# Kernel tuning notes

Hardware: AMD Instinct MI355X
Metric: run time of the kernel (lower is better)

## Reference

```python
import jax, jax.numpy as jnp
import numpy as np

B, S, D, H, HD = 2, 2048, 1024, 16, 64
LN_EPS = 1e-6


def setup_inputs() -> dict:
    key = jax.random.key(0)
    ks = jax.random.split(key, 4)
    x = jax.random.normal(ks[0], (B, S, D), dtype=jnp.float32)
    ln_scale = jnp.ones((D,), jnp.float32)
    ln_bias = jnp.zeros((D,), jnp.float32)
    w_qkv = jax.random.normal(ks[1], (D, H, 3 * HD), jnp.float32) * (D ** -0.5)
    b_qkv = jnp.zeros((H, 3 * HD), jnp.float32)
    w_out = jax.random.normal(ks[2], (H, HD, D), jnp.float32) * ((H * HD) ** -0.5)
    b_out = jnp.zeros((D,), jnp.float32)
    # causal mask, broadcastable to weights shape [B, H, q, k]
    mask = jnp.tril(jnp.ones((S, S), dtype=bool))[None, None, :, :]
    return {"x": x, "ln_scale": ln_scale, "ln_bias": ln_bias,
            "w_qkv": w_qkv, "b_qkv": b_qkv, "w_out": w_out, "b_out": b_out,
            "mask": mask}


def _attention_block(x, ln_scale, ln_bias, w_qkv, b_qkv, w_out, b_out, mask):
    # Pre-LayerNorm
    mu = jnp.mean(x, axis=-1, keepdims=True)
    var = jnp.mean(jnp.square(x - mu), axis=-1, keepdims=True)
    xn = (x - mu) * jax.lax.rsqrt(var + LN_EPS) * ln_scale + ln_bias
    # QKV projection: [B,S,D] x [D,H,3*hd] -> [B,S,H,3*hd]
    qkv = jnp.einsum('bsd,dhf->bshf', xn, w_qkv) + b_qkv
    q, k, v = jnp.split(qkv, 3, axis=-1)  # each [B,S,H,hd]
    # scaled dot-product attention in float32 (softmax_dtype)
    scale = HD ** -0.5
    qf = (q * scale).astype(jnp.float32)
    kf = k.astype(jnp.float32)
    weights = jnp.einsum('bqhd,bkhd->bhqk', qf, kf)  # [B,H,S,S]
    weights = jnp.where(mask, weights, jnp.finfo(jnp.float32).min)
    weights = jax.nn.softmax(weights, axis=-1).astype(x.dtype)
    attn = jnp.einsum('bhqk,bkhd->bqhd', weights, v)  # [B,S,H,hd]
    # output projection, contracting (H, hd)
    out = jnp.einsum('bqhd,hdf->bqf', attn, w_out) + b_out  # [B,S,D]
    return out


def reference(x, ln_scale, ln_bias, w_qkv, b_qkv, w_out, b_out, mask):
    return _attention_block(x, ln_scale, ln_bias, w_qkv, b_qkv, w_out, b_out, mask)
```

## Files before the change

kernel.cpp:

```cpp
#include <hip/hip_runtime.h>
#include <hip/hip_bf16.h>
#include <stdint.h>

#define B_ 2
#define S_ 2048
#define D_ 1024
#define H_ 16
#define HD_ 64
#define M_ (B_*S_)
#define NQKV_ (H_*3*HD_)

typedef __attribute__((ext_vector_type(8))) short short8;
typedef __attribute__((ext_vector_type(4))) float f32x4;
typedef unsigned short u16;
typedef unsigned int u32;

__device__ __forceinline__ u16 f2b(float f){
  u32 u = __float_as_uint(f);
  u32 r = (u + 0x7FFFu + ((u >> 16) & 1u)) >> 16;
  return (u16)r;
}

__device__ __forceinline__ float exp2v(float x){
  float r; asm("v_exp_f32 %0, %1" : "=v"(r) : "v"(x)); return r;
}

__device__ __forceinline__ void gl_lds16(const void* g, void* l){
  __builtin_amdgcn_global_load_lds(
      (const __attribute__((address_space(1))) void*)g,
      (__attribute__((address_space(3))) void*)l, 16, 0, 0);
}

__global__ __launch_bounds__(256) void prep_kernel(
    const float* __restrict__ x, const float* __restrict__ gam,
    const float* __restrict__ bet, u16* __restrict__ xn,
    const float* __restrict__ wqkv, u16* __restrict__ wqkvT,
    const float* __restrict__ wout, u16* __restrict__ woutT){
  int bid = blockIdx.x;
  __shared__ float tile[64][65];
  if(bid < M_){
    int row = bid;
    const float4* xr = (const float4*)(x + (size_t)row * D_);
    float4 v = xr[threadIdx.x];
    float s = v.x + v.y + v.z + v.w;
    float q = v.x*v.x + v.y*v.y + v.z*v.z + v.w*v.w;
    #pragma unroll
    for(int o = 32; o > 0; o >>= 1){ s += __shfl_down(s, o); q += __shfl_down(q, o); }
    float* red = &tile[0][0];
    int w = threadIdx.x >> 6, lane = threadIdx.x & 63;
    if(lane == 0){ red[w] = s; red[4+w] = q; }
    __syncthreads();
    float st = red[0]+red[1]+red[2]+red[3];
    float qt = red[4]+red[5]+red[6]+red[7];
    float mu = st * (1.0f / D_);
    float inv = rsqrtf(qt * (1.0f / D_) - mu*mu + 1e-6f);
    float4 g = ((const float4*)gam)[threadIdx.x];
    float4 b = ((const float4*)bet)[threadIdx.x];
    ushort4 o4;
    o4.x = f2b((v.x-mu)*inv*g.x + b.x);
    o4.y = f2b((v.y-mu)*inv*g.y + b.y);
    o4.z = f2b((v.z-mu)*inv*g.z + b.z);
    o4.w = f2b((v.w-mu)*inv*g.w + b.w);
    ((ushort4*)(xn + (size_t)row * D_))[threadIdx.x] = o4;
    return;
  }
  const float* src; u16* dst; int C, cx, ry;
  if(bid < M_ + (NQKV_/64)*(D_/64)){
    int idx = bid - M_;
    cx = idx % (NQKV_/64); ry = idx / (NQKV_/64);
    src = wqkv; dst = wqkvT; C = NQKV_;
  } else {
    int idx = bid - M_ - (NQKV_/64)*(D_/64);
    cx = idx % (D_/64); ry = idx / (D_/64);
    src = wout; dst = woutT; C = D_;
  }
  const int R = D_;
  int tx = threadIdx.x & 63, ty = threadIdx.x >> 6;
  int r0 = ry * 64, c0 = cx * 64;
  #pragma unroll
  for(int i = 0; i < 16; i++){
    int r = ty*16 + i;
    tile[r][tx] = src[(size_t)(r0+r)*C + c0 + tx];
  }
  __syncthreads();
  #pragma unroll
  for(int i = 0; i < 16; i++){
    int r = ty*16 + i;
    dst[(size_t)(c0+r)*R + r0 + tx] = f2b(tile[tx][r]);
  }
}

__global__ __launch_bounds__(512, 1) void gemm256_kernel(const u16* __restrict__ A,
    const u16* __restrict__ Bt, const float* __restrict__ bias,
    u16* __restrict__ o0, u16* __restrict__ o1, u16* __restrict__ o2t){
  constexpr int K_ = 1024;
  __shared__ __align__(16) char smem[114688];
  int tid = threadIdx.x, w = tid >> 6, lane = tid & 63;
  int wm = w >> 1, wn = w & 1;
  int bid = blockIdx.y * gridDim.x + blockIdx.x;
  int nwg = gridDim.x * gridDim.y;
  int cpx = nwg >> 3;
  int swz = (bid & 7) * cpx + (bid >> 3);
  int m0 = (swz / gridDim.x) * 256, n0 = (swz % gridDim.x) * 192;

  f32x4 z = {0.f, 0.f, 0.f, 0.f};
  f32x4 acc[4][6];
  #pragma unroll
  for(int r = 0; r < 4; r++)
    #pragma unroll
    for(int c = 0; c < 6; c++) acc[r][c] = z;

  int srow8 = tid >> 3;
  int sch = (tid & 7) ^ (srow8 & 7);
  auto STAGE_A = [&](int buf, int half, int kt){
    #pragma unroll
    for(int l = 0; l < 2; l++){
      int row = half*128 + l*64 + srow8;
      gl_lds16(A + (size_t)(m0 + row)*K_ + kt*64 + sch*8,
               smem + buf*32768 + half*16384 + l*8192 + tid*16);
    }
  };
  auto STAGE_B3 = [&](int slot, int third, int kt){
    int row = third*64 + srow8;
    gl_lds16(Bt + (size_t)(n0 + row)*K_ + kt*64 + sch*8,
             smem + 65536 + slot*24576 + third*8192 + tid*16);
  };

  int ln15 = lane & 15, g = lane >> 4;
  int co0 = ((g    ) ^ (ln15 & 7)) * 16;
  int co1 = ((4 + g) ^ (ln15 & 7)) * 16;
  auto LDA = [&](int buf, int r, int k)->short8{
    int row = wm*64 + r*16 + ln15;
    return *(const short8*)(smem + buf*32768 + row*128 + (k ? co1 : co0));
  };
  auto LDB = [&](int slot, int c, int k)->short8{
    int row = wn*96 + c*16 + ln15;
    return *(const short8*)(smem + 65536 + slot*24576 + row*128 + (k ? co1 : co0));
  };
  #define BAR()   __builtin_amdgcn_s_barrier()
  #define LGKM0() do{ asm volatile("s_waitcnt lgkmcnt(0)" ::: "memory"); \
                      __builtin_amdgcn_sched_barrier(0); }while(0)
  #define MF(r_, c_, a_, b_) acc[r_][c_] = __builtin_amdgcn_mfma_f32_16x16x32_bf16(a_, b_, acc[r_][c_], 0, 0, 0)

  constexpr int nk = K_ / 64;
  STAGE_A(0, 0, 0); STAGE_A(0, 1, 0);
  STAGE_B3(0, 0, 0); STAGE_B3(0, 1, 0); STAGE_B3(0, 2, 0);
  STAGE_B3(1, 0, 1); STAGE_B3(1, 1, 1); STAGE_B3(1, 2, 1);
  asm volatile("s_waitcnt vmcnt(3)" ::: "memory");
  __builtin_amdgcn_sched_barrier(0);
  BAR();

  #pragma unroll 2
  for(int t = 0; t < nk; t++){
    int buf = t & 1;
    int kA = (t + 1 < nk) ? t + 1 : nk - 1;
    int kB = (t + 2 < nk) ? t + 2 : nk - 1;
    short8 a[4][2], b01[2][2], b23[2][2], b45[2][2];
    #pragma unroll
    for(int r = 0; r < 4; r++){ a[r][0] = LDA(buf, r, 0); a[r][1] = LDA(buf, r, 1); }
    #pragma unroll
    for(int c = 0; c < 2; c++){ b01[c][0] = LDB(buf, c, 0); b01[c][1] = LDB(buf, c, 1); }
    STAGE_A(buf ^ 1, 0, kA);
    BAR(); LGKM0();
    __builtin_amdgcn_s_setprio(1);
    #pragma unroll
    for(int r = 0; r < 4; r++)
      #pragma unroll
      for(int c = 0; c < 2; c++){ MF(r, c, a[r][0], b01[c][0]); MF(r, c, a[r][1], b01[c][1]); }
    __builtin_amdgcn_s_setprio(0);
    BAR();
    #pragma unroll
    for(int c = 0; c < 2; c++){ b23[c][0] = LDB(buf, c + 2, 0); b23[c][1] = LDB(buf, c + 2, 1); }
    STAGE_A(buf ^ 1, 1, kA);
    BAR(); LGKM0();
    __builtin_amdgcn_s_setprio(1);
    #pragma unroll
    for(int r = 0; r < 4; r++)
      #pragma unroll
      for(int c = 0; c < 2; c++){ MF(r, c+2, a[r][0], b23[c][0]); MF(r, c+2, a[r][1], b23[c][1]); }
    __builtin_amdgcn_s_setprio(0);
    BAR();
    #pragma unroll
    for(int c = 0; c < 2; c++){ b45[c][0] = LDB(buf, c + 4, 0); b45[c][1] = LDB(buf, c + 4, 1); }
    BAR(); LGKM0();
    __builtin_amdgcn_s_setprio(1);
    #pragma unroll
    for(int r = 0; r < 4; r++){ MF(r, 4, a[r][0], b45[0][0]); MF(r, 4, a[r][1], b45[0][1]); }
    __builtin_amdgcn_s_setprio(0);
    BAR();
    STAGE_B3(buf, 0, kB); STAGE_B3(buf, 1, kB); STAGE_B3(buf, 2, kB);
    BAR();
    __builtin_amdgcn_s_setprio(1);
    #pragma unroll
    for(int r = 0; r < 4; r++){ MF(r, 5, a[r][0], b45[1][0]); MF(r, 5, a[r][1], b45[1][1]); }
    __builtin_amdgcn_s_setprio(0);
    asm volatile("s_waitcnt vmcnt(3)" ::: "memory");
    __builtin_amdgcn_sched_barrier(0);
    BAR();
  }
  #undef BAR
  #undef LGKM0
  #undef MF

  int h = n0 / 192;
  #pragma unroll
  for(int r = 0; r < 4; r++){
    #pragma unroll
    for(int c = 0; c < 6; c++){
      #pragma unroll
      for(int q = 0; q < 4; q++){
        int row = m0 + wm*64 + r*16 + g*4 + q;
        int rr = wn*96 + c*16 + ln15;
        float v = acc[r][c][q] + bias[h*192 + rr];
        int b = row >> 11, s = row & (S_ - 1);
        if(rr < 64){
          o0[((size_t)(b*H_ + h)*S_ + s)*HD_ + rr] = f2b(v * 0.180336884f);
        } else if(rr < 128){
          o1[((size_t)(b*H_ + h)*S_ + s)*HD_ + rr - 64] = f2b(v);
        } else {
          o2t[((size_t)(b*H_ + h)*HD_ + rr - 128)*S_ + s] = f2b(v);
        }
      }
    }
  }
}

__global__ __launch_bounds__(256) void gemm_kernel(const u16* __restrict__ A,
    const u16* __restrict__ Bt, const float* __restrict__ bias,
    float* __restrict__ out, int K, int N){
  __shared__ u16 As[2][128*32];
  __shared__ u16 Bs[2][128*32];
  int tid = threadIdx.x, w = tid >> 6, lane = tid & 63;
  int bid = blockIdx.y * gridDim.x + blockIdx.x;
  int nwg = gridDim.x * gridDim.y;
  int cpx = nwg >> 3;
  int swz = (bid & 7) * cpx + (bid >> 3);
  int m0 = (swz / gridDim.x) * 128, n0 = (swz % gridDim.x) * 128;
  int wm = w >> 1, wn = w & 1;
  f32x4 z = {0.f, 0.f, 0.f, 0.f};
  f32x4 acc[4][4];
  #pragma unroll
  for(int r = 0; r < 4; r++)
    #pragma unroll
    for(int c = 0; c < 4; c++) acc[r][c] = z;
  int srow = lane >> 2, sch = (lane & 3) * 8;
  const u16* Ag = A + (size_t)m0 * K + (size_t)srow * K + sch;
  const u16* Bg = Bt + (size_t)n0 * K + (size_t)srow * K + sch;

  auto STAGE = [&](int buf, int kt){
    #pragma unroll
    for(int i = 0; i < 2; i++){
      int rb = w*32 + i*16;
      gl_lds16(Ag + (size_t)rb*K + kt, &As[buf][rb*32]);
      gl_lds16(Bg + (size_t)rb*K + kt, &Bs[buf][rb*32]);
    }
  };

  int nk = K >> 5;
  STAGE(0, 0);
  asm volatile("s_waitcnt vmcnt(0)" ::: "memory");
  __builtin_amdgcn_sched_barrier(0);
  __builtin_amdgcn_s_barrier();
  for(int t = 0; t < nk; t++){
    int cur = t & 1;
    if(t + 1 < nk){
      STAGE(cur ^ 1, (t + 1) * 32);
      asm volatile("s_waitcnt vmcnt(4)" ::: "memory");
    } else {
      asm volatile("s_waitcnt vmcnt(0)" ::: "memory");
    }
    __builtin_amdgcn_sched_barrier(0);
    __builtin_amdgcn_s_barrier();
    int kc = (lane >> 4) * 8;
    int ar = wm*64 + (lane & 15);
    int bc = wn*64 + (lane & 15);
    short8 af[4], bfr[4];
    #pragma unroll
    for(int r = 0; r < 4; r++) af[r] = *(const short8*)&As[cur][(ar + r*16)*32 + kc];
    #pragma unroll
    for(int c = 0; c < 4; c++) bfr[c] = *(const short8*)&Bs[cur][(bc + c*16)*32 + kc];
    __builtin_amdgcn_s_setprio(1);
    #pragma unroll
    for(int r = 0; r < 4; r++)
      #pragma unroll
      for(int c = 0; c < 4; c++)
        acc[r][c] = __builtin_amdgcn_mfma_f32_16x16x32_bf16(af[r], bfr[c], acc[r][c], 0, 0, 0);
    __builtin_amdgcn_s_setprio(0);
    asm volatile("" ::: "memory");
    __builtin_amdgcn_s_barrier();
  }

  #pragma unroll
  for(int r = 0; r < 4; r++){
    #pragma unroll
    for(int c = 0; c < 4; c++){
      #pragma unroll
      for(int q = 0; q < 4; q++){
        int row = m0 + wm*64 + r*16 + (lane >> 4)*4 + q;
        int col = n0 + wn*64 + c*16 + (lane & 15);
        out[(size_t)row * N + col] = acc[r][c][q] + bias[col];
      }
    }
  }
}


template<int HALF>
__device__ __forceinline__ void compute_tile(
    const char* KsB, const char* VsB, char* Pw, const short8* qf,
    f32x4* o, float& m_run, float& l_run, bool diag, int lane, int wr){
  constexpr int KB0 = (HALF == 1) ? 2 : 0;
  constexpr int KBN = (HALF == -1) ? 4 : 2;
  f32x4 z = {0.f, 0.f, 0.f, 0.f};
  f32x4 sf[4];
  __builtin_amdgcn_s_setprio(1);
  #pragma unroll
  for(int kb = KB0; kb < KB0 + KBN; kb++){
    f32x4 acc = z;
    #pragma unroll
    for(int c = 0; c < 2; c++){
      int row = kb*16 + (lane & 15);
      int kc16 = (lane >> 4) + c*4;
      short8 kf = *(const short8*)(KsB + row*128 + ((kc16 ^ (row & 7)) * 16));
      acc = __builtin_amdgcn_mfma_f32_16x16x32_bf16(kf, qf[c], acc, 0, 0, 0);
    }
    sf[kb] = acc;
  }
  __builtin_amdgcn_s_setprio(0);
  if(diag){
    int qo = wr*16 + (lane & 15);
    #pragma unroll
    for(int kb = KB0; kb < KB0 + KBN; kb++)
      #pragma unroll
      for(int r = 0; r < 4; r++){
        int kvo = kb*16 + (lane >> 4)*4 + r;
        if(kvo > qo) sf[kb][r] = -1e30f;
      }
  }
  int g = lane >> 4;
  float pmax = -1e28f;
  #pragma unroll
  for(int kb = KB0; kb < KB0 + KBN; kb++)
    pmax = fmaxf(pmax, fmaxf(fmaxf(sf[kb][0], sf[kb][1]), fmaxf(sf[kb][2], sf[kb][3])));
  pmax = fmaxf(pmax, __shfl_xor(pmax, 16));
  pmax = fmaxf(pmax, __shfl_xor(pmax, 32));
  if(!__all(pmax <= m_run + 8.f)){
    float mn = fmaxf(m_run, pmax);
    float al = exp2v(m_run - mn);
    m_run = mn;
    l_run *= al;
    float alr[4];
    #pragma unroll
    for(int r = 0; r < 4; r++) alr[r] = __shfl(al, g*4 + r);
    #pragma unroll
    for(int n = 0; n < 4; n++)
      #pragma unroll
      for(int r = 0; r < 4; r++) o[n][r] *= alr[r];
  }
  float p[4][4];
  float sum = 0.f;
  #pragma unroll
  for(int kb = KB0; kb < KB0 + KBN; kb++){
    #pragma unroll
    for(int r = 0; r < 4; r++) p[kb][r] = exp2v(sf[kb][r] - m_run);
    sum += (p[kb][0]+p[kb][1]) + (p[kb][2]+p[kb][3]);
  }
  sum += __shfl_xor(sum, 16);
  sum += __shfl_xor(sum, 32);
  l_run += sum;
  int qrow = lane & 15;
  #pragma unroll
  for(int kb = KB0; kb < KB0 + KBN; kb++){
    u32 lo, hi;
    asm("v_cvt_pk_bf16_f32 %0, %1, %2" : "=v"(lo) : "v"(p[kb][0]), "v"(p[kb][1]));
    asm("v_cvt_pk_bf16_f32 %0, %1, %2" : "=v"(hi) : "v"(p[kb][2]), "v"(p[kb][3]));
    uint2 pk; pk.x = lo; pk.y = hi;
    int byt = (qrow*128 + kb*32 + g*8) ^ ((qrow & 7) << 4);
    *(uint2*)(Pw + byt) = pk;
  }
  constexpr int C0 = (HALF == 1) ? 1 : 0;
  constexpr int C1 = (HALF == 0) ? 0 : 1;
  __builtin_amdgcn_s_setprio(1);
  #pragma unroll
  for(int c = C0; c <= C1; c++){
    int prow = lane & 15;
    int kb16 = ((lane >> 4) + c*4) * 16;
    short8 pa = *(const short8*)(Pw + ((prow*128 + kb16) ^ ((prow & 7) << 4)));
    #pragma unroll
    for(int n = 0; n < 4; n++){
      int vrow = n*16 + (lane & 15);
      int kc16 = (lane >> 4) + c*4;
      short8 vf = *(const short8*)(VsB + vrow*128 + ((kc16 ^ (vrow & 7)) * 16));
      o[n] = __builtin_amdgcn_mfma_f32_16x16x32_bf16(pa, vf, o[n], 0, 0, 0);
    }
  }
  __builtin_amdgcn_s_setprio(0);
}

__global__ __launch_bounds__(512) void attn_kernel(const u16* __restrict__ Q,
    const u16* __restrict__ Kb, const u16* __restrict__ Vt, u16* __restrict__ O){
  __shared__ __align__(16) char smem[49152];
  char* PsBase = smem + 32768;
  int tid = threadIdx.x, w = tid >> 6, lane = tid & 63;
  int wr = w & 3, role = w >> 2;
  int L = blockIdx.x;
  int pi = (L >> 3) & 15;
  int bh = (L & 7) + 8 * (L >> 7);
  const int NT = S_ / 64;
  int ta = pi, tb = NT - 1 - pi;
  const u16* Qg = Q + (size_t)bh * S_ * HD_;
  const u16* Kg = Kb + (size_t)bh * S_ * HD_;
  const u16* Vg = Vt + (size_t)bh * HD_ * S_;
  int b = bh >> 4, h = bh & 15;

  short8 qb[2], qa[2];
  {
    int rb_ = tb*64 + wr*16 + (lane & 15);
    #pragma unroll
    for(int c = 0; c < 2; c++)
      qb[c] = *(const short8*)(Qg + (size_t)rb_*HD_ + (lane >> 4)*8 + c*32);
    if(role == 1){
      int ra_ = ta*64 + wr*16 + (lane & 15);
      #pragma unroll
      for(int c = 0; c < 2; c++)
        qa[c] = *(const short8*)(Qg + (size_t)ra_*HD_ + (lane >> 4)*8 + c*32);
    }
  }
  f32x4 z = {0.f, 0.f, 0.f, 0.f};
  f32x4 o[4];
  float m_run = -1e30f, l_run = 0.f;
  #pragma unroll
  for(int i = 0; i < 4; i++) o[i] = z;
  int svrow = lane >> 3, scb = lane & 7;

  auto STAGE = [&](int buf, int kt){
    int kv0 = kt * 64;
    int rowblk = w * 8;
    int row = rowblk + svrow;
    int cbs = scb ^ (row & 7);
    gl_lds16(Kg + (size_t)(kv0 + row)*HD_ + cbs*8, smem + buf*8192 + rowblk*128);
    gl_lds16(Vg + (size_t)row*S_ + kv0 + cbs*8, smem + 16384 + buf*8192 + rowblk*128);
  };

  STAGE(0, 0);
  asm volatile("s_waitcnt vmcnt(0)" ::: "memory");
  __builtin_amdgcn_sched_barrier(0);
  __builtin_amdgcn_s_barrier();
  int cur = 0;
  char* Pw = PsBase + w*2048;
  for(int kt = 0; kt <= tb; kt++){
    if(kt < tb){
      STAGE(cur ^ 1, kt + 1);
      asm volatile("s_waitcnt vmcnt(2)" ::: "memory");
    } else {
      asm volatile("s_waitcnt vmcnt(0)" ::: "memory");
    }
    __builtin_amdgcn_sched_barrier(0);
    __builtin_amdgcn_s_barrier();
    const char* KsB = (const char*)(smem + cur*8192);
    const char* VsB = (const char*)(smem + 16384 + cur*8192);
    if(role == 0){
      if(kt <= ta) compute_tile<-1>(KsB, VsB, Pw, qb, o, m_run, l_run, false, lane, wr);
      else         compute_tile<0>(KsB, VsB, Pw, qb, o, m_run, l_run, kt == tb, lane, wr);
    } else {
      if(kt <= ta){
        compute_tile<-1>(KsB, VsB, Pw, qa, o, m_run, l_run, kt == ta, lane, wr);
        if(kt == ta){
          float linv = 1.f / l_run;
          float invr[4];
          #pragma unroll
          for(int r = 0; r < 4; r++) invr[r] = __shfl(linv, (lane >> 4)*4 + r);
          #pragma unroll
          for(int n = 0; n < 4; n++)
            #pragma unroll
            for(int r = 0; r < 4; r++){
              int s = ta*64 + wr*16 + (lane >> 4)*4 + r;
              int hd = n*16 + (lane & 15);
              O[(((size_t)(b*S_ + s))*H_ + h)*HD_ + hd] = f2b(o[n][r] * invr[r]);
            }
          m_run = -1e30f; l_run = 0.f;
          #pragma unroll
          for(int i = 0; i < 4; i++) o[i] = z;
        }
      } else {
        compute_tile<1>(KsB, VsB, Pw, qb, o, m_run, l_run, kt == tb, lane, wr);
      }
    }
    asm volatile("" ::: "memory");
    __builtin_amdgcn_s_barrier();
    cur ^= 1;
  }

  float* Mg = (float*)smem + wr*1072;
  if(role == 1){
    #pragma unroll
    for(int n = 0; n < 4; n++)
      #pragma unroll
      for(int r = 0; r < 4; r++)
        Mg[((lane >> 4)*4 + r)*65 + n*16 + (lane & 15)] = o[n][r];
    if(lane < 16){ Mg[1040 + lane] = m_run; Mg[1056 + lane] = l_run; }
  }
  __syncthreads();
  if(role == 0){
    float F1[4], F2[4], den[4];
    #pragma unroll
    for(int r = 0; r < 4; r++){
      int row = (lane >> 4)*4 + r;
      float m1r = __shfl(m_run, row);
      float l1r = __shfl(l_run, row);
      float m2r = Mg[1040 + row];
      float l2r = Mg[1056 + row];
      float mm = fmaxf(m1r, m2r);
      F1[r] = exp2v(m1r - mm);
      F2[r] = exp2v(m2r - mm);
      den[r] = 1.f / (l1r*F1[r] + l2r*F2[r]);
    }
    #pragma unroll
    for(int n = 0; n < 4; n++)
      #pragma unroll
      for(int r = 0; r < 4; r++){
        int row = (lane >> 4)*4 + r;
        float o2 = Mg[row*65 + n*16 + (lane & 15)];
        float val = (o[n][r]*F1[r] + o2*F2[r]) * den[r];
        int s = tb*64 + wr*16 + row;
        int hd = n*16 + (lane & 15);
        O[(((size_t)(b*S_ + s))*H_ + h)*HD_ + hd] = f2b(val);
      }
  }
}

extern "C" void kernel_launch(void* const* d_in, const int* in_sizes, int n_in,
                              void* d_out, int out_size, void* d_ws, size_t ws_size,
                              hipStream_t stream){
  (void)in_sizes; (void)n_in; (void)out_size; (void)ws_size;
  const float* x    = (const float*)d_in[0];
  const float* gam  = (const float*)d_in[1];
  const float* bet  = (const float*)d_in[2];
  const float* wqkv = (const float*)d_in[3];
  const float* bqkv = (const float*)d_in[4];
  const float* wout = (const float*)d_in[5];
  const float* bout = (const float*)d_in[6];
  char* ws = (char*)d_ws;
  u16* xn    = (u16*)(ws);
  u16* wqkvT = (u16*)(ws + 8388608);
  u16* woutT = (u16*)(ws + 8388608 + 6291456);
  u16* Qb    = (u16*)(ws + 16777216);
  u16* Kb    = (u16*)(ws + 16777216 + 8388608);
  u16* Vt    = (u16*)(ws + 16777216 + 2*8388608);
  u16* attnb = xn;
  float* out = (float*)d_out;

  prep_kernel<<<dim3(M_ + (NQKV_/64)*(D_/64) + (D_/64)*(D_/64)), dim3(256), 0, stream>>>(
      x, gam, bet, xn, wqkv, wqkvT, wout, woutT);
  gemm256_kernel<<<dim3(NQKV_/192, M_/256), dim3(512), 0, stream>>>(xn, wqkvT, bqkv, Qb, Kb, Vt);
  attn_kernel<<<dim3(512), dim3(512), 0, stream>>>(Qb, Kb, Vt, attnb);
  gemm_kernel<<<dim3(D_/128, M_/128), dim3(256), 0, stream>>>(attnb, woutT, bout, out, D_, D_);
}
```

Baseline: 115.3 us.

## Replace paired causal q-tile blocks with one q-tile per block, split KV halves

The attention kernel no longer pairs a short and a long causal query tile per block. Each block now handles a single 64-row query tile, with the two wave groups splitting every 64-key KV tile into halves, and the grid doubles to 1024 blocks. Blocks are ordered longest-first, so dynamic scheduling has to do the load balancing. This removes the mid-loop epilogue and the divergent role logic, but it loads each KV tile once per query tile instead of once per pair and halves the MFMA work per barrier.

```diff
diff --git a/kernel.cpp b/kernel.cpp
--- a/kernel.cpp
+++ b/kernel.cpp
@@ -310,12 +310,11 @@
     const char* KsB, const char* VsB, char* Pw, const short8* qf,
     f32x4* o, float& m_run, float& l_run, bool diag, int lane, int wr){
   constexpr int KB0 = (HALF == 1) ? 2 : 0;
-  constexpr int KBN = (HALF == -1) ? 4 : 2;
   f32x4 z = {0.f, 0.f, 0.f, 0.f};
   f32x4 sf[4];
   __builtin_amdgcn_s_setprio(1);
   #pragma unroll
-  for(int kb = KB0; kb < KB0 + KBN; kb++){
+  for(int kb = KB0; kb < KB0 + 2; kb++){
     f32x4 acc = z;
     #pragma unroll
     for(int c = 0; c < 2; c++){
@@ -330,7 +329,7 @@
   if(diag){
     int qo = wr*16 + (lane & 15);
     #pragma unroll
-    for(int kb = KB0; kb < KB0 + KBN; kb++)
+    for(int kb = KB0; kb < KB0 + 2; kb++)
       #pragma unroll
       for(int r = 0; r < 4; r++){
         int kvo = kb*16 + (lane >> 4)*4 + r;
@@ -340,7 +339,7 @@
   int g = lane >> 4;
   float pmax = -1e28f;
   #pragma unroll
-  for(int kb = KB0; kb < KB0 + KBN; kb++)
+  for(int kb = KB0; kb < KB0 + 2; kb++)
     pmax = fmaxf(pmax, fmaxf(fmaxf(sf[kb][0], sf[kb][1]), fmaxf(sf[kb][2], sf[kb][3])));
   pmax = fmaxf(pmax, __shfl_xor(pmax, 16));
   pmax = fmaxf(pmax, __shfl_xor(pmax, 32));
@@ -360,7 +359,7 @@
   float p[4][4];
   float sum = 0.f;
   #pragma unroll
-  for(int kb = KB0; kb < KB0 + KBN; kb++){
+  for(int kb = KB0; kb < KB0 + 2; kb++){
     #pragma unroll
     for(int r = 0; r < 4; r++) p[kb][r] = exp2v(sf[kb][r] - m_run);
     sum += (p[kb][0]+p[kb][1]) + (p[kb][2]+p[kb][3]);
@@ -370,7 +369,7 @@
   l_run += sum;
   int qrow = lane & 15;
   #pragma unroll
-  for(int kb = KB0; kb < KB0 + KBN; kb++){
+  for(int kb = KB0; kb < KB0 + 2; kb++){
     u32 lo, hi;
     asm("v_cvt_pk_bf16_f32 %0, %1, %2" : "=v"(lo) : "v"(p[kb][0]), "v"(p[kb][1]));
     asm("v_cvt_pk_bf16_f32 %0, %1, %2" : "=v"(hi) : "v"(p[kb][2]), "v"(p[kb][3]));
@@ -378,11 +377,9 @@
     int byt = (qrow*128 + kb*32 + g*8) ^ ((qrow & 7) << 4);
     *(uint2*)(Pw + byt) = pk;
   }
-  constexpr int C0 = (HALF == 1) ? 1 : 0;
-  constexpr int C1 = (HALF == 0) ? 0 : 1;
   __builtin_amdgcn_s_setprio(1);
-  #pragma unroll
-  for(int c = C0; c <= C1; c++){
+  {
+    constexpr int c = HALF;
     int prow = lane & 15;
     int kb16 = ((lane >> 4) + c*4) * 16;
     short8 pa = *(const short8*)(Pw + ((prow*128 + kb16) ^ ((prow & 7) << 4)));
@@ -404,27 +401,19 @@
   int tid = threadIdx.x, w = tid >> 6, lane = tid & 63;
   int wr = w & 3, role = w >> 2;
   int L = blockIdx.x;
-  int pi = (L >> 3) & 15;
-  int bh = (L & 7) + 8 * (L >> 7);
-  const int NT = S_ / 64;
-  int ta = pi, tb = NT - 1 - pi;
+  int qt = 31 - (L >> 5);
+  int bh = (L & 7) + 8 * ((L >> 3) & 3);
   const u16* Qg = Q + (size_t)bh * S_ * HD_;
   const u16* Kg = Kb + (size_t)bh * S_ * HD_;
   const u16* Vg = Vt + (size_t)bh * HD_ * S_;
   int b = bh >> 4, h = bh & 15;
 
-  short8 qb[2], qa[2];
+  short8 qf[2];
   {
-    int rb_ = tb*64 + wr*16 + (lane & 15);
+    int rq = qt*64 + wr*16 + (lane & 15);
     #pragma unroll
     for(int c = 0; c < 2; c++)
-      qb[c] = *(const short8*)(Qg + (size_t)rb_*HD_ + (lane >> 4)*8 + c*32);
-    if(role == 1){
-      int ra_ = ta*64 + wr*16 + (lane & 15);
-      #pragma unroll
-      for(int c = 0; c < 2; c++)
-        qa[c] = *(const short8*)(Qg + (size_t)ra_*HD_ + (lane >> 4)*8 + c*32);
-    }
+      qf[c] = *(const short8*)(Qg + (size_t)rq*HD_ + (lane >> 4)*8 + c*32);
   }
   f32x4 z = {0.f, 0.f, 0.f, 0.f};
   f32x4 o[4];
@@ -448,8 +437,8 @@
   __builtin_amdgcn_s_barrier();
   int cur = 0;
   char* Pw = PsBase + w*2048;
-  for(int kt = 0; kt <= tb; kt++){
-    if(kt < tb){
+  for(int kt = 0; kt <= qt; kt++){
+    if(kt < qt){
       STAGE(cur ^ 1, kt + 1);
       asm volatile("s_waitcnt vmcnt(2)" ::: "memory");
     } else {
@@ -459,33 +448,8 @@
     __builtin_amdgcn_s_barrier();
     const char* KsB = (const char*)(smem + cur*8192);
     const char* VsB = (const char*)(smem + 16384 + cur*8192);
-    if(role == 0){
-      if(kt <= ta) compute_tile<-1>(KsB, VsB, Pw, qb, o, m_run, l_run, false, lane, wr);
-      else         compute_tile<0>(KsB, VsB, Pw, qb, o, m_run, l_run, kt == tb, lane, wr);
-    } else {
-      if(kt <= ta){
-        compute_tile<-1>(KsB, VsB, Pw, qa, o, m_run, l_run, kt == ta, lane, wr);
-        if(kt == ta){
-          float linv = 1.f / l_run;
-          float invr[4];
-          #pragma unroll
-          for(int r = 0; r < 4; r++) invr[r] = __shfl(linv, (lane >> 4)*4 + r);
-          #pragma unroll
-          for(int n = 0; n < 4; n++)
-            #pragma unroll
-            for(int r = 0; r < 4; r++){
-              int s = ta*64 + wr*16 + (lane >> 4)*4 + r;
-              int hd = n*16 + (lane & 15);
-              O[(((size_t)(b*S_ + s))*H_ + h)*HD_ + hd] = f2b(o[n][r] * invr[r]);
-            }
-          m_run = -1e30f; l_run = 0.f;
-          #pragma unroll
-          for(int i = 0; i < 4; i++) o[i] = z;
-        }
-      } else {
-        compute_tile<1>(KsB, VsB, Pw, qb, o, m_run, l_run, kt == tb, lane, wr);
-      }
-    }
+    if(role == 0) compute_tile<0>(KsB, VsB, Pw, qf, o, m_run, l_run, kt == qt, lane, wr);
+    else          compute_tile<1>(KsB, VsB, Pw, qf, o, m_run, l_run, kt == qt, lane, wr);
     asm volatile("" ::: "memory");
     __builtin_amdgcn_s_barrier();
     cur ^= 1;
@@ -522,7 +486,7 @@
         int row = (lane >> 4)*4 + r;
         float o2 = Mg[row*65 + n*16 + (lane & 15)];
         float val = (o[n][r]*F1[r] + o2*F2[r]) * den[r];
-        int s = tb*64 + wr*16 + row;
+        int s = qt*64 + wr*16 + row;
         int hd = n*16 + (lane & 15);
         O[(((size_t)(b*S_ + s))*H_ + h)*HD_ + hd] = f2b(val);
       }
@@ -553,6 +517,6 @@
   prep_kernel<<<dim3(M_ + (NQKV_/64)*(D_/64) + (D_/64)*(D_/64)), dim3(256), 0, stream>>>(
       x, gam, bet, xn, wqkv, wqkvT, wout, woutT);
   gemm256_kernel<<<dim3(NQKV_/192, M_/256), dim3(512), 0, stream>>>(xn, wqkvT, bqkv, Qb, Kb, Vt);
-  attn_kernel<<<dim3(512), dim3(512), 0, stream>>>(Qb, Kb, Vt, attnb);
+  attn_kernel<<<dim3(32*B_*H_), dim3(512), 0, stream>>>(Qb, Kb, Vt, attnb);
   gemm_kernel<<<dim3(D_/128, M_/128), dim3(256), 0, stream>>>(attnb, woutT, bout, out, D_, D_);
 }
```

New measurement: 109.2 us. 1.06x faster.
